# Optimization experiments

Hardware: AMD Instinct MI355X
Metric: run time of the kernel (lower is better)

Reference implementation:

```python
import jax, jax.numpy as jnp
import numpy as np
from jax import lax

B = 256
WIDTH = 64
STRUCT = [512, 1024, 1024, 1000]
N_LAYERS = len(STRUCT) - 2  # LSTM layers (last pair is the classifier)


def setup_inputs() -> dict:
    key = jax.random.key(0)
    ks = list(jax.random.split(key, 2 + 4 * N_LAYERS))
    inp = {"x": jax.random.normal(ks[0], (B, STRUCT[0] * WIDTH), jnp.float32)}
    ki = 1
    for j in range(N_LAYERS):
        n_x, n_h = STRUCT[j], STRUCT[j + 1]
        n_v = n_h + n_x  # variants == 0: concat(h_prev, x)
        std = np.float32(np.sqrt(2.0 / (n_v + n_h)))
        for g in ["F", "I", "C", "O"]:
            inp[f"{g}{j}"] = jax.random.normal(ks[ki], (n_v, n_h), jnp.float32) * std
            ki += 1
        for g in ["bf", "bi", "bc", "bo"]:
            inp[f"{g}{j}"] = jnp.zeros((n_h,), jnp.float32)
    n_x, n_h = STRUCT[-2], STRUCT[-1]
    std = np.float32(np.sqrt(2.0 / (n_x + n_h)))
    inp["W"] = jax.random.normal(ks[ki], (n_x, n_h), jnp.float32) * std
    inp["b"] = jnp.zeros((n_h,), jnp.float32)
    return inp


def _lstm_forward(x, params, W, b):
    # x: [B, WIDTH*n_in] -> xs: [WIDTH, B, n_in] (tf.split along axis 1)
    bsz = x.shape[0]
    xs = x.reshape(bsz, WIDTH, STRUCT[0]).transpose(1, 0, 2)

    def step(carry, x_t):
        new_carry = []
        h = x_t
        for j, (F, I, C, O, bf, bi, bc, bo) in enumerate(params):
            c_f, h_f = carry[j]
            # variants==0: x_in = concat([h_prev, x]); k==0 sliced-weight path
            # equals zero h_prev/c_prev, so zero-init state is faithful.
            x_in = jnp.concatenate([h_f, h], axis=1)  # [B, n_h + n_x]
            f = jax.nn.sigmoid(x_in @ F + bf)
            i = jax.nn.sigmoid(x_in @ I + bi)
            c = f * c_f + i * jnp.tanh(x_in @ C + bc)
            o = jax.nn.sigmoid(x_in @ O + bo)
            h = o * jnp.tanh(c)
            new_carry.append((c, h))
        return tuple(new_carry), None

    init = tuple(
        (jnp.zeros((bsz, STRUCT[j + 1]), x.dtype), jnp.zeros((bsz, STRUCT[j + 1]), x.dtype))
        for j in range(N_LAYERS)
    )
    carry, _ = lax.scan(step, init, xs)
    h_last = carry[-1][1]  # top layer hidden at final timestep
    logits = h_last @ W + b
    pred = jax.nn.softmax(logits, axis=-1)
    return logits, pred


def reference(x, F0, I0, C0, O0, bf0, bi0, bc0, bo0,
              F1, I1, C1, O1, bf1, bi1, bc1, bo1, W, b):
    params = [
        (F0, I0, C0, O0, bf0, bi0, bc0, bo0),
        (F1, I1, C1, O1, bf1, bi1, bc1, bo1),
    ]
    return _lstm_forward(x, params, W, b)
```

## Files before the change

### kernel.cpp

```cpp
#include <hip/hip_runtime.h>
#include <hip/hip_bf16.h>


typedef short  bf16x8 __attribute__((ext_vector_type(8)));
typedef float  f32x4  __attribute__((ext_vector_type(4)));

#define NHID   1024
#define NBATCH 256
#define NBLK   256
#define HSZE   (NBATCH * NHID)

__device__ __forceinline__ unsigned short f2b(float f) {
    unsigned int u = __builtin_bit_cast(unsigned int, f);
    unsigned int r = (u + 0x7FFFu + ((u >> 16) & 1u)) >> 16;
    return (unsigned short)r;
}
__device__ __forceinline__ float sigmoidf_(float x) {
    return 1.0f / (1.0f + __expf(-x));
}
__device__ __forceinline__ float tanhf_(float x) {
    return 1.0f - 2.0f / (__expf(2.0f * x) + 1.0f);
}

__global__ __launch_bounds__(256)
void transpose_w_kernel(const float* __restrict__ w0, const float* __restrict__ w1,
                        const float* __restrict__ w2, const float* __restrict__ w3,
                        unsigned short* __restrict__ dst, int nv) {
    __shared__ unsigned short t[64][65];
    const int gate = blockIdx.z;
    const float* src = (gate == 0) ? w0 : (gate == 1) ? w1 : (gate == 2) ? w2 : w3;
    const int kt = blockIdx.x * 64;
    const int nt = blockIdx.y * 64;
    const int tid = threadIdx.x;
    const int rr = tid >> 6;
    const int cc = tid & 63;
    #pragma unroll
    for (int p = 0; p < 16; ++p) {
        const int row = p * 4 + rr;
        t[cc][row] = f2b(src[(size_t)(kt + row) * NHID + nt + cc]);
    }
    __syncthreads();
    #pragma unroll
    for (int p = 0; p < 16; ++p) {
        const int row = p * 4 + rr;
        dst[((size_t)gate * NHID + nt + row) * nv + kt + cc] = t[row][cc];
    }
}

__global__ __launch_bounds__(256)
void cvt_x_frag_kernel(const float* __restrict__ x, unsigned short* __restrict__ xb) {
    const int t  = blockIdx.x;
    const int mg = blockIdx.y;
    const int g  = threadIdx.x >> 6;
    const int l  = threadIdx.x & 63;
    const int row = l & 15, ko = l >> 4;
    const float* src = x + (size_t)(mg * 16 + row) * 32768 + t * 512 + ko * 8;
    unsigned short* dst = xb + ((size_t)t * 256 * 512) + ((size_t)mg * 16 * 64 + l) * 8;
    #pragma unroll
    for (int i = 0; i < 4; ++i) {
        const int c = g * 4 + i;
        const float4 v0 = *(const float4*)(src + (size_t)c * 32);
        const float4 v1 = *(const float4*)(src + (size_t)c * 32 + 4);
        ushort4 o0, o1;
        o0.x = f2b(v0.x); o0.y = f2b(v0.y); o0.z = f2b(v0.z); o0.w = f2b(v0.w);
        o1.x = f2b(v1.x); o1.y = f2b(v1.y); o1.z = f2b(v1.z); o1.w = f2b(v1.w);
        *(ushort4*)(dst + (size_t)c * 512)     = o0;
        *(ushort4*)(dst + (size_t)c * 512 + 4) = o1;
    }
}

__device__ __forceinline__ void layer_sync(unsigned* bar, unsigned gen,
                                           int layer, int lb) {
    __syncthreads();
    if (threadIdx.x == 0) {
        __builtin_amdgcn_fence(__ATOMIC_RELEASE, "agent");
        unsigned* base = bar + layer * 96;
        unsigned* grp  = base + (lb & 3) * 16;
        unsigned* stg  = base + 64;
        unsigned* gctr = base + 80;
        unsigned* octr = bar + (layer ? 80 : 176);
        if (__hip_atomic_fetch_add(grp, 1u, __ATOMIC_RELAXED, __HIP_MEMORY_SCOPE_AGENT)
                == gen * 32u + 31u) {
            if (__hip_atomic_fetch_add(stg, 1u, __ATOMIC_RELAXED, __HIP_MEMORY_SCOPE_AGENT)
                    == gen * 4u + 3u)
                __hip_atomic_store(gctr, gen + 1u, __ATOMIC_RELAXED, __HIP_MEMORY_SCOPE_AGENT);
        }
        while (__hip_atomic_load(gctr, __ATOMIC_RELAXED, __HIP_MEMORY_SCOPE_AGENT) <= gen)
            __builtin_amdgcn_s_sleep(2);
        if (layer == 1) {
            while (__hip_atomic_load(octr, __ATOMIC_RELAXED, __HIP_MEMORY_SCOPE_AGENT) <= gen)
                __builtin_amdgcn_s_sleep(2);
        } else if (gen >= 2) {
            while (__hip_atomic_load(octr, __ATOMIC_RELAXED, __HIP_MEMORY_SCOPE_AGENT) < gen - 1u)
                __builtin_amdgcn_s_sleep(2);
        }
        __builtin_amdgcn_fence(__ATOMIC_ACQUIRE, "agent");
    }
    __syncthreads();
}

__global__ __launch_bounds__(1024, 4)
void lstm_persist_kernel(const unsigned short* __restrict__ wt0,
                         const unsigned short* __restrict__ wt1,
                         const unsigned short* __restrict__ xb,
                         const float* __restrict__ bf0, const float* __restrict__ bi0,
                         const float* __restrict__ bc0, const float* __restrict__ bo0,
                         const float* __restrict__ bf1, const float* __restrict__ bi1,
                         const float* __restrict__ bc1, const float* __restrict__ bo1,
                         unsigned short* __restrict__ h0b,
                         unsigned short* __restrict__ h1b,
                         float* __restrict__ h1f,
                         unsigned* __restrict__ bar) {
    __shared__ __align__(16) unsigned short lw[65536];

    const int tid  = threadIdx.x;
    const int lane = tid & 63;
    const int w    = tid >> 6;
    const int c15  = lane & 15;
    const int kg   = lane >> 4;
    const int b    = blockIdx.x;
    const int layer = (b >> 3) & 1;
    const int lb    = ((b >> 4) << 3) | (b & 7);

    const unsigned short* wt = layer ? wt1 : wt0;
    const int NV  = layer ? 2048 : 1536;
    const int NCW = NV >> 5;

    #pragma unroll
    for (int i = 0; i < 4; ++i) {
        const int c = w + i * 16;
        if (c < NCW) {
            #pragma unroll
            for (int rt = 0; rt < 2; ++rt) {
                const int R   = rt * 16 + c15;
                const int g   = R >> 3;
                const int hid = 8 * lb + (R & 7);
                const int k   = c * 32 + kg * 8;
                *(bf16x8*)(lw + ((size_t)(c * 2 + rt) * 64 + lane) * 8) =
                    *(const bf16x8*)(wt + ((size_t)g * NHID + hid) * NV + k);
            }
        }
    }

    f32x4 biasv[2];
    {
        const float* bp[4];
        if (layer) { bp[0] = bf1; bp[1] = bi1; bp[2] = bc1; bp[3] = bo1; }
        else       { bp[0] = bf0; bp[1] = bi0; bp[2] = bc0; bp[3] = bo0; }
        #pragma unroll
        for (int rt = 0; rt < 2; ++rt)
            #pragma unroll
            for (int j = 0; j < 4; ++j) {
                const int R = rt * 16 + kg * 4 + j;
                biasv[rt][j] = bp[R >> 3][8 * lb + (R & 7)];
            }
    }
    __syncthreads();

    float cs[2] = {0.f, 0.f};
    unsigned gen = 0;

    const int rot_h  = (b >> 3) & 31;
    const int rot_xL = layer ? rot_h : ((b >> 4) & 15);

    const int hb4  = 4 * (kg & 1);
    const int jsel = (kg >> 1) ? 2 : 0;
    const int hp   = hb4 + jsel;
    const int mrow = 16 * w + c15;
    const int chw  = lb >> 2;
    const int kow  = lb & 3;
    const size_t hoff = (((size_t)w * 32 + chw) * 64 + kow * 16 + c15) * 8 + hp;

    auto step = [&](const int NX, const int rot_x,
                    const unsigned short* bh, const unsigned short* bx,
                    unsigned short* hout, float* hfout) {
        f32x4 acc0 = biasv[0], acc1 = biasv[1];
        const unsigned short* ph = bh + ((size_t)w * 32 * 64 + lane) * 8;
        const unsigned short* px = bx + ((size_t)w * NX * 64 + lane) * 8;

        #pragma unroll 8
        for (int i = 0; i < 32; ++i) {
            const int cc = (i + rot_h) & 31;
            const bf16x8 vb  = *(const bf16x8*)(ph + (size_t)cc * 512);
            const bf16x8 va0 = *(const bf16x8*)(lw + ((size_t)(cc * 2)     * 64 + lane) * 8);
            const bf16x8 va1 = *(const bf16x8*)(lw + ((size_t)(cc * 2 + 1) * 64 + lane) * 8);
            acc0 = __builtin_amdgcn_mfma_f32_16x16x32_bf16(va0, vb, acc0, 0, 0, 0);
            acc1 = __builtin_amdgcn_mfma_f32_16x16x32_bf16(va1, vb, acc1, 0, 0, 0);
        }
        #pragma unroll 8
        for (int i = 0; i < NX; ++i) {
            const int cc = (i + rot_x) & (NX - 1);
            const bf16x8 vb  = *(const bf16x8*)(px + (size_t)cc * 512);
            const bf16x8 va0 = *(const bf16x8*)(lw + ((size_t)((32 + cc) * 2)     * 64 + lane) * 8);
            const bf16x8 va1 = *(const bf16x8*)(lw + ((size_t)((32 + cc) * 2 + 1) * 64 + lane) * 8);
            acc0 = __builtin_amdgcn_mfma_f32_16x16x32_bf16(va0, vb, acc0, 0, 0, 0);
            acc1 = __builtin_amdgcn_mfma_f32_16x16x32_bf16(va1, vb, acc1, 0, 0, 0);
        }

        f32x4 racc0, racc1;
        #pragma unroll
        for (int j = 0; j < 4; ++j) {
            racc0[j] = __shfl_xor(acc0[j], 32);
            racc1[j] = __shfl_xor(acc1[j], 32);
        }

        float hv[2];
        #pragma unroll
        for (int jj = 0; jj < 2; ++jj) {
            const int j = jsel + jj;
            float fsv, isv, csv, osv;
            if (kg < 2) { fsv = acc0[j];  isv = racc0[j]; csv = acc1[j];  osv = racc1[j]; }
            else        { fsv = racc0[j]; isv = acc0[j];  csv = racc1[j]; osv = acc1[j];  }
            const float fv = sigmoidf_(fsv);
            const float iv = sigmoidf_(isv);
            const float cv = tanhf_(csv);
            const float ov = sigmoidf_(osv);
            const float ccv = fv * cs[jj] + iv * cv;
            const float hh  = ov * tanhf_(ccv);
            cs[jj] = ccv;
            hv[jj] = hh;
        }
        const unsigned hbp = (unsigned)f2b(hv[0]) | ((unsigned)f2b(hv[1]) << 16);
        *reinterpret_cast<unsigned*>(hout + hoff) = hbp;
        if (hfout) {
            float2 hf; hf.x = hv[0]; hf.y = hv[1];
            *reinterpret_cast<float2*>(hfout + (size_t)mrow * NHID + 8 * lb + hp) = hf;
        }
    };

    for (int t = 0; t <= 64; ++t) {
        if (layer == 0) {
            if (t < 64) {
                step(16, rot_xL,
                     h0b + (size_t)((t + 3) & 3) * HSZE,
                     xb + (size_t)t * 256 * 512,
                     h0b + (size_t)(t & 3) * HSZE, nullptr);
            }
        } else {
            if (t >= 1) {
                const int u = t - 1;
                step(32, rot_xL,
                     h1b + (size_t)((u + 1) & 1) * HSZE,
                     h0b + (size_t)(u & 3) * HSZE,
                     h1b + (size_t)(u & 1) * HSZE,
                     (u == 63) ? h1f : nullptr);
            }
        }
        if (t < 64) {
            layer_sync(bar, gen, layer, lb);
            ++gen;
        }
    }
}

__global__ __launch_bounds__(256)
void classifier_kernel(const float* __restrict__ h, const float* __restrict__ W,
                       const float* __restrict__ b, float* __restrict__ logits) {
    __shared__ float hs[4 * 1024];
    const int tid = threadIdx.x;
    const int m0 = blockIdx.y * 4;
    const int n  = blockIdx.x * 256 + tid;
    #pragma unroll
    for (int i = 0; i < 16; ++i)
        hs[i * 256 + tid] = h[(size_t)m0 * NHID + i * 256 + tid];
    __syncthreads();
    if (n < 1000) {
        float a0 = 0.f, a1 = 0.f, a2 = 0.f, a3 = 0.f;
        #pragma unroll 8
        for (int k = 0; k < NHID; ++k) {
            const float wv = W[(size_t)k * 1000 + n];
            a0 = fmaf(hs[k], wv, a0);
            a1 = fmaf(hs[1024 + k], wv, a1);
            a2 = fmaf(hs[2048 + k], wv, a2);
            a3 = fmaf(hs[3072 + k], wv, a3);
        }
        const float bv = b[n];
        logits[(size_t)(m0 + 0) * 1000 + n] = a0 + bv;
        logits[(size_t)(m0 + 1) * 1000 + n] = a1 + bv;
        logits[(size_t)(m0 + 2) * 1000 + n] = a2 + bv;
        logits[(size_t)(m0 + 3) * 1000 + n] = a3 + bv;
    }
}

__global__ void softmax_kernel(const float* __restrict__ logits, float* __restrict__ pred) {
    __shared__ float red[256];
    const int m = blockIdx.x;
    const int t = threadIdx.x;
    const float* lr = logits + (size_t)m * 1000;
    float mx = -3.4e38f;
    for (int i = t; i < 1000; i += 256) mx = fmaxf(mx, lr[i]);
    red[t] = mx; __syncthreads();
    for (int off = 128; off > 0; off >>= 1) {
        if (t < off) red[t] = fmaxf(red[t], red[t + off]);
        __syncthreads();
    }
    mx = red[0];
    __syncthreads();
    float sm = 0.0f;
    for (int i = t; i < 1000; i += 256) sm += __expf(lr[i] - mx);
    red[t] = sm; __syncthreads();
    for (int off = 128; off > 0; off >>= 1) {
        if (t < off) red[t] += red[t + off];
        __syncthreads();
    }
    const float inv = 1.0f / red[0];
    for (int i = t; i < 1000; i += 256)
        pred[(size_t)m * 1000 + i] = __expf(lr[i] - mx) * inv;
}

extern "C" void kernel_launch(void* const* d_in, const int* in_sizes, int n_in,
                              void* d_out, int out_size, void* d_ws, size_t ws_size,
                              hipStream_t stream) {
    (void)in_sizes; (void)n_in; (void)out_size; (void)ws_size;
    const float* x = (const float*)d_in[0];
    const float* W0[4] = {(const float*)d_in[1], (const float*)d_in[2], (const float*)d_in[3], (const float*)d_in[4]};
    const float* B0[4] = {(const float*)d_in[5], (const float*)d_in[6], (const float*)d_in[7], (const float*)d_in[8]};
    const float* W1[4] = {(const float*)d_in[9], (const float*)d_in[10], (const float*)d_in[11], (const float*)d_in[12]};
    const float* B1[4] = {(const float*)d_in[13], (const float*)d_in[14], (const float*)d_in[15], (const float*)d_in[16]};
    const float* Wc = (const float*)d_in[17];
    const float* bc = (const float*)d_in[18];
    float* out = (float*)d_out;

    char* ws = (char*)d_ws;
    size_t off = 0;
    auto alloc = [&](size_t bytes) -> char* {
        char* p = ws + off;
        off += (bytes + 255) & ~(size_t)255;
        return p;
    };
    unsigned short* wt0 = (unsigned short*)alloc((size_t)4 * NHID * 1536 * 2);
    unsigned short* wt1 = (unsigned short*)alloc((size_t)4 * NHID * 2048 * 2);
    unsigned short* xb  = (unsigned short*)alloc((size_t)NBATCH * 64 * 512 * 2);
    char* hstates = ws + off;
    unsigned short* h0b = (unsigned short*)alloc((size_t)4 * HSZE * 2);
    unsigned short* h1b = (unsigned short*)alloc((size_t)2 * HSZE * 2);
    size_t hstate_bytes = (size_t)((char*)h1b + (size_t)2 * HSZE * 2 - hstates);
    float* h1f = (float*)alloc((size_t)HSZE * 4);
    unsigned* bar = (unsigned*)alloc(1024);

    hipMemsetAsync(hstates, 0, hstate_bytes, stream);
    hipMemsetAsync(bar, 0, 1024, stream);

    transpose_w_kernel<<<dim3(1536 / 64, 16, 4), 256, 0, stream>>>(
        W0[0], W0[1], W0[2], W0[3], wt0, 1536);
    transpose_w_kernel<<<dim3(2048 / 64, 16, 4), 256, 0, stream>>>(
        W1[0], W1[1], W1[2], W1[3], wt1, 2048);
    cvt_x_frag_kernel<<<dim3(64, 16), 256, 0, stream>>>(x, xb);

    lstm_persist_kernel<<<NBLK, 1024, 0, stream>>>(
        wt0, wt1, xb,
        B0[0], B0[1], B0[2], B0[3],
        B1[0], B1[1], B1[2], B1[3],
        h0b, h1b, h1f, bar);

    classifier_kernel<<<dim3(4, 64), 256, 0, stream>>>(h1f, Wc, bc, out);
    softmax_kernel<<<NBATCH, 256, 0, stream>>>(out, out + (size_t)NBATCH * 1000);
}
```

Baseline: 1.406 ms.

## Switch LSTM recurrence to 32x32x16 MFMA with 512-thread blocks

Replaces the pair of 16x16x32 bf16 MFMAs per k-chunk with a single 32x32x16 MFMA covering all 32 gate rows of the block. Each wave now owns 32 batch rows, so blocks drop to 8 waves. The h/x fragment layouts, the x conversion kernel and the weight staging in LDS are rewritten to match. The aim is fewer instructions per step, no cross-lane shuffle to gather the gates, and wider h stores, at the cost of fewer waves to hide the latency of global h loads.

New measurement: 1.493 ms. +6.1%, slower.

```diff
diff --git a/kernel.cpp b/kernel.cpp
--- a/kernel.cpp
+++ b/kernel.cpp
@@ -4,6 +4,7 @@
 
 typedef short  bf16x8 __attribute__((ext_vector_type(8)));
 typedef float  f32x4  __attribute__((ext_vector_type(4)));
+typedef float  f32x16 __attribute__((ext_vector_type(16)));
 
 #define NHID   1024
 #define NBATCH 256
@@ -51,21 +52,23 @@
 void cvt_x_frag_kernel(const float* __restrict__ x, unsigned short* __restrict__ xb) {
     const int t  = blockIdx.x;
     const int mg = blockIdx.y;
-    const int g  = threadIdx.x >> 6;
     const int l  = threadIdx.x & 63;
-    const int row = l & 15, ko = l >> 4;
-    const float* src = x + (size_t)(mg * 16 + row) * 32768 + t * 512 + ko * 8;
-    unsigned short* dst = xb + ((size_t)t * 256 * 512) + ((size_t)mg * 16 * 64 + l) * 8;
+    const int q  = threadIdx.x >> 6;
+    const int col = l & 31, kh2 = l >> 5;
+    const float* srcm = x + (size_t)(mg * 32 + col) * 32768 + t * 512;
+    unsigned short* dstb = xb + (((size_t)t * 8 + mg) * 32 * 64 + l) * 8;
     #pragma unroll
-    for (int i = 0; i < 4; ++i) {
-        const int c = g * 4 + i;
-        const float4 v0 = *(const float4*)(src + (size_t)c * 32);
-        const float4 v1 = *(const float4*)(src + (size_t)c * 32 + 4);
+    for (int i = 0; i < 8; ++i) {
+        const int kc = q * 8 + i;
+        const int k  = kc * 16 + kh2 * 8;
+        const float4 v0 = *(const float4*)(srcm + k);
+        const float4 v1 = *(const float4*)(srcm + k + 4);
         ushort4 o0, o1;
         o0.x = f2b(v0.x); o0.y = f2b(v0.y); o0.z = f2b(v0.z); o0.w = f2b(v0.w);
         o1.x = f2b(v1.x); o1.y = f2b(v1.y); o1.z = f2b(v1.z); o1.w = f2b(v1.w);
-        *(ushort4*)(dst + (size_t)c * 512)     = o0;
-        *(ushort4*)(dst + (size_t)c * 512 + 4) = o1;
+        unsigned short* d = dstb + (size_t)kc * 512;
+        *(ushort4*)(d)     = o0;
+        *(ushort4*)(d + 4) = o1;
     }
 }
 
@@ -99,7 +102,7 @@
     __syncthreads();
 }
 
-__global__ __launch_bounds__(1024, 4)
+__global__ __launch_bounds__(512, 2)
 void lstm_persist_kernel(const unsigned short* __restrict__ wt0,
                          const unsigned short* __restrict__ wt1,
                          const unsigned short* __restrict__ xb,
@@ -116,130 +119,109 @@
     const int tid  = threadIdx.x;
     const int lane = tid & 63;
     const int w    = tid >> 6;
-    const int c15  = lane & 15;
-    const int kg   = lane >> 4;
+    const int col  = lane & 31;
+    const int hi   = lane >> 5;
     const int b    = blockIdx.x;
     const int layer = (b >> 3) & 1;
     const int lb    = ((b >> 4) << 3) | (b & 7);
 
     const unsigned short* wt = layer ? wt1 : wt0;
     const int NV  = layer ? 2048 : 1536;
-    const int NCW = NV >> 5;
-
-    #pragma unroll
-    for (int i = 0; i < 4; ++i) {
-        const int c = w + i * 16;
-        if (c < NCW) {
-            #pragma unroll
-            for (int rt = 0; rt < 2; ++rt) {
-                const int R   = rt * 16 + c15;
-                const int g   = R >> 3;
-                const int hid = 8 * lb + (R & 7);
-                const int k   = c * 32 + kg * 8;
-                *(bf16x8*)(lw + ((size_t)(c * 2 + rt) * 64 + lane) * 8) =
-                    *(const bf16x8*)(wt + ((size_t)g * NHID + hid) * NV + k);
-            }
-        }
-    }
-
-    f32x4 biasv[2];
+    const int NCW = NV >> 4;
+    const int NX  = layer ? 64 : 32;
+
+    {
+        const int R   = lane & 31;
+        const int g   = R >> 3;
+        const int hid = 8 * lb + (R & 7);
+        const unsigned short* s = wt + ((size_t)g * NHID + hid) * NV + hi * 8;
+        #pragma unroll
+        for (int i = 0; i < 16; ++i) {
+            const int kc = w + i * 8;
+            if (kc < NCW)
+                *(bf16x8*)(lw + ((size_t)kc * 64 + lane) * 8) =
+                    *(const bf16x8*)(s + kc * 16);
+        }
+    }
+
+    f32x16 biasv;
     {
         const float* bp[4];
         if (layer) { bp[0] = bf1; bp[1] = bi1; bp[2] = bc1; bp[3] = bo1; }
         else       { bp[0] = bf0; bp[1] = bi0; bp[2] = bc0; bp[3] = bo0; }
         #pragma unroll
-        for (int rt = 0; rt < 2; ++rt)
-            #pragma unroll
-            for (int j = 0; j < 4; ++j) {
-                const int R = rt * 16 + kg * 4 + j;
-                biasv[rt][j] = bp[R >> 3][8 * lb + (R & 7)];
-            }
-    }
-    __syncthreads();
-
-    float cs[2] = {0.f, 0.f};
+        for (int g = 0; g < 4; ++g) {
+            const float4 v = *(const float4*)(bp[g] + 8 * lb + 4 * hi);
+            biasv[4 * g + 0] = v.x; biasv[4 * g + 1] = v.y;
+            biasv[4 * g + 2] = v.z; biasv[4 * g + 3] = v.w;
+        }
+    }
+    __syncthreads();
+
+    float cs[4] = {0.f, 0.f, 0.f, 0.f};
     unsigned gen = 0;
 
-    const int rot_h  = (b >> 3) & 31;
-    const int rot_xL = layer ? rot_h : ((b >> 4) & 15);
-
-    const int hb4  = 4 * (kg & 1);
-    const int jsel = (kg >> 1) ? 2 : 0;
-    const int hp   = hb4 + jsel;
-    const int mrow = 16 * w + c15;
-    const int chw  = lb >> 2;
-    const int kow  = lb & 3;
-    const size_t hoff = (((size_t)w * 32 + chw) * 64 + kow * 16 + c15) * 8 + hp;
-
-    auto step = [&](const int NX, const int rot_x,
+    const int rot_h  = (b >> 3) & 63;
+    const int rot_xL = layer ? ((b >> 3) & 63) : ((b >> 4) & 31);
+
+    const size_t hoff = (((size_t)w * 64 + (lb >> 1)) * 64 + (lb & 1) * 32 + col) * 8 + 4 * hi;
+    const int mrow = 32 * w + col;
+
+    auto step = [&](const int NXc, const int rot_x,
                     const unsigned short* bh, const unsigned short* bx,
                     unsigned short* hout, float* hfout) {
-        f32x4 acc0 = biasv[0], acc1 = biasv[1];
-        const unsigned short* ph = bh + ((size_t)w * 32 * 64 + lane) * 8;
-        const unsigned short* px = bx + ((size_t)w * NX * 64 + lane) * 8;
+        f32x16 acc = biasv;
+        const unsigned short* ph = bh + ((size_t)w * 64 * 64 + lane) * 8;
+        const unsigned short* px = bx + ((size_t)w * NXc * 64 + lane) * 8;
 
         #pragma unroll 8
-        for (int i = 0; i < 32; ++i) {
-            const int cc = (i + rot_h) & 31;
-            const bf16x8 vb  = *(const bf16x8*)(ph + (size_t)cc * 512);
-            const bf16x8 va0 = *(const bf16x8*)(lw + ((size_t)(cc * 2)     * 64 + lane) * 8);
-            const bf16x8 va1 = *(const bf16x8*)(lw + ((size_t)(cc * 2 + 1) * 64 + lane) * 8);
-            acc0 = __builtin_amdgcn_mfma_f32_16x16x32_bf16(va0, vb, acc0, 0, 0, 0);
-            acc1 = __builtin_amdgcn_mfma_f32_16x16x32_bf16(va1, vb, acc1, 0, 0, 0);
+        for (int i = 0; i < 64; ++i) {
+            const int kc = (i + rot_h) & 63;
+            const bf16x8 vb = *(const bf16x8*)(ph + (size_t)kc * 512);
+            const bf16x8 va = *(const bf16x8*)(lw + ((size_t)kc * 64 + lane) * 8);
+            acc = __builtin_amdgcn_mfma_f32_32x32x16_bf16(va, vb, acc, 0, 0, 0);
         }
         #pragma unroll 8
-        for (int i = 0; i < NX; ++i) {
-            const int cc = (i + rot_x) & (NX - 1);
-            const bf16x8 vb  = *(const bf16x8*)(px + (size_t)cc * 512);
-            const bf16x8 va0 = *(const bf16x8*)(lw + ((size_t)((32 + cc) * 2)     * 64 + lane) * 8);
-            const bf16x8 va1 = *(const bf16x8*)(lw + ((size_t)((32 + cc) * 2 + 1) * 64 + lane) * 8);
-            acc0 = __builtin_amdgcn_mfma_f32_16x16x32_bf16(va0, vb, acc0, 0, 0, 0);
-            acc1 = __builtin_amdgcn_mfma_f32_16x16x32_bf16(va1, vb, acc1, 0, 0, 0);
-        }
-
-        f32x4 racc0, racc1;
+        for (int i = 0; i < NXc; ++i) {
+            const int kc = (i + rot_x) & (NXc - 1);
+            const bf16x8 vb = *(const bf16x8*)(px + (size_t)kc * 512);
+            const bf16x8 va = *(const bf16x8*)(lw + ((size_t)(64 + kc) * 64 + lane) * 8);
+            acc = __builtin_amdgcn_mfma_f32_32x32x16_bf16(va, vb, acc, 0, 0, 0);
+        }
+
+        float hv[4];
         #pragma unroll
         for (int j = 0; j < 4; ++j) {
-            racc0[j] = __shfl_xor(acc0[j], 32);
-            racc1[j] = __shfl_xor(acc1[j], 32);
-        }
-
-        float hv[2];
-        #pragma unroll
-        for (int jj = 0; jj < 2; ++jj) {
-            const int j = jsel + jj;
-            float fsv, isv, csv, osv;
-            if (kg < 2) { fsv = acc0[j];  isv = racc0[j]; csv = acc1[j];  osv = racc1[j]; }
-            else        { fsv = racc0[j]; isv = acc0[j];  csv = racc1[j]; osv = acc1[j];  }
-            const float fv = sigmoidf_(fsv);
-            const float iv = sigmoidf_(isv);
-            const float cv = tanhf_(csv);
-            const float ov = sigmoidf_(osv);
-            const float ccv = fv * cs[jj] + iv * cv;
-            const float hh  = ov * tanhf_(ccv);
-            cs[jj] = ccv;
-            hv[jj] = hh;
-        }
-        const unsigned hbp = (unsigned)f2b(hv[0]) | ((unsigned)f2b(hv[1]) << 16);
-        *reinterpret_cast<unsigned*>(hout + hoff) = hbp;
+            const float fv = sigmoidf_(acc[j]);
+            const float iv = sigmoidf_(acc[4 + j]);
+            const float cv = tanhf_(acc[8 + j]);
+            const float ov = sigmoidf_(acc[12 + j]);
+            const float cc = fv * cs[j] + iv * cv;
+            const float hh = ov * tanhf_(cc);
+            cs[j] = cc;
+            hv[j] = hh;
+        }
+        ushort4 hb;
+        hb.x = f2b(hv[0]); hb.y = f2b(hv[1]); hb.z = f2b(hv[2]); hb.w = f2b(hv[3]);
+        *reinterpret_cast<ushort4*>(hout + hoff) = hb;
         if (hfout) {
-            float2 hf; hf.x = hv[0]; hf.y = hv[1];
-            *reinterpret_cast<float2*>(hfout + (size_t)mrow * NHID + 8 * lb + hp) = hf;
+            float4 hf; hf.x = hv[0]; hf.y = hv[1]; hf.z = hv[2]; hf.w = hv[3];
+            *reinterpret_cast<float4*>(hfout + (size_t)mrow * NHID + 8 * lb + 4 * hi) = hf;
         }
     };
 
     for (int t = 0; t <= 64; ++t) {
         if (layer == 0) {
             if (t < 64) {
-                step(16, rot_xL,
+                step(32, rot_xL,
                      h0b + (size_t)((t + 3) & 3) * HSZE,
-                     xb + (size_t)t * 256 * 512,
+                     xb + (size_t)t * 8 * 32 * 64 * 8,
                      h0b + (size_t)(t & 3) * HSZE, nullptr);
             }
         } else {
             if (t >= 1) {
                 const int u = t - 1;
-                step(32, rot_xL,
+                step(64, rot_xL,
                      h1b + (size_t)((u + 1) & 1) * HSZE,
                      h0b + (size_t)(u & 3) * HSZE,
                      h1b + (size_t)(u & 1) * HSZE,
@@ -345,9 +327,9 @@
         W0[0], W0[1], W0[2], W0[3], wt0, 1536);
     transpose_w_kernel<<<dim3(2048 / 64, 16, 4), 256, 0, stream>>>(
         W1[0], W1[1], W1[2], W1[3], wt1, 2048);
-    cvt_x_frag_kernel<<<dim3(64, 16), 256, 0, stream>>>(x, xb);
-
-    lstm_persist_kernel<<<NBLK, 1024, 0, stream>>>(
+    cvt_x_frag_kernel<<<dim3(64, 8), 256, 0, stream>>>(x, xb);
+
+    lstm_persist_kernel<<<NBLK, 512, 0, stream>>>(
         wt0, wt1, xb,
         B0[0], B0[1], B0[2], B0[3],
         B1[0], B1[1], B1[2], B1[3],
```
